# Kernel tuning notes

Measured on AMD Instinct MI355X. Metric: run time of the kernel, lower is better.

Reference implementation:

```python
import jax, jax.numpy as jnp
import numpy as np

DT = 0.001  # integration time step (forward arg dt in the original module)


def force_fn(x):
    # Harmonic well stand-in for the user-supplied force function.
    return -x


def _nh_step(x, v, alpha, kT, mass, Q):
    """One Nose-Hoover step, exactly mirroring the recompute block in backward()."""
    ndof = x.shape[-1]
    v2 = (v * v).sum(-1)
    alpha = alpha + (DT / 4) * (v2 - ndof * kT) / Q
    v = v * jnp.exp(-alpha[..., None] * (DT / 2))
    v2 = (v * v).sum(-1)
    alpha = alpha + (DT / 4) * (v2 - ndof * kT) / Q
    v = v + (DT / 2) * force_fn(x) / mass
    x = x + DT * v
    v = v + (DT / 2) * force_fn(x) / mass
    v2 = (v * v).sum(-1)
    alpha = alpha + (DT / 4) * (v2 - ndof * kT) / Q
    v = v * jnp.exp(-alpha[..., None] * (DT / 2))
    v2 = (v * v).sum(-1)
    alpha = alpha + (DT / 4) * (v2 - ndof * kT) / Q
    return x, v, alpha


def setup_inputs() -> dict:
    key = jax.random.key(0)
    k1, k2 = jax.random.split(key)
    B, D = 4096, 64  # batch of systems, degrees of freedom per system
    return {
        "x0": jax.random.normal(k1, (B, D), jnp.float32),
        "v0": jax.random.normal(k2, (B, D), jnp.float32),
        "alpha0": jnp.zeros((B,), jnp.float32),
        "kT": jnp.ones((), jnp.float32),
        "mass": jnp.ones((), jnp.float32),
        "Q": jnp.ones((), jnp.float32),
        "n_steps": 1000,
        "store_every": 10,
    }


def reference(x0, v0, alpha0, kT, mass, Q, n_steps, store_every):
    n_chunks = n_steps // store_every  # assume divisibility (1000 / 10)

    def inner(c, _):
        x, v, a = c
        return _nh_step(x, v, a, kT, mass, Q), None

    def chunk(c, _):
        c, _ = jax.lax.scan(inner, c, None, length=store_every)
        return c, (c[0], c[1])  # snapshot (x, v) every store_every steps

    _, (xs, vs) = jax.lax.scan(chunk, (x0, v0, alpha0), None, length=n_chunks)
    traj_x = jnp.concatenate([x0[None], xs], axis=0)  # [n_steps//store_every + 1, B, D]
    traj_v = jnp.concatenate([v0[None], vs], axis=0)
    return traj_x, traj_v
```

## Files before the change

### kernel.cpp

```cpp
#include <hip/hip_runtime.h>

#define DT 0.001f

typedef float f4 __attribute__((ext_vector_type(4)));

template<int CTRL>
__device__ __forceinline__ float dpp_add(float v) {
    int r = __builtin_amdgcn_update_dpp(0, __float_as_int(v), CTRL, 0xf, 0xf, false);
    return v + __int_as_float(r);
}

__device__ __forceinline__ float reduce16(float t) {
    t = dpp_add<0x121>(t);
    t = dpp_add<0x122>(t);
    t = dpp_add<0x124>(t);
    t = dpp_add<0x128>(t);
    return t;
}

__device__ __forceinline__ float sumsq(const f4 a) {
    return (a.x * a.x + a.y * a.y) + (a.z * a.z + a.w * a.w);
}
__device__ __forceinline__ float dot4(const f4 a, const f4 b) {
    return (a.x * b.x + a.y * b.y) + (a.z * b.z + a.w * b.w);
}

template<int SE>
__device__ __forceinline__ void run(
    f4& x, f4& u, float& sv, float& al_mcE,
    float& Sxx, float& Sxv, float& Svv,
    int n_chunks, int se_rt,
    float c, float c2, float c2E,
    float A11, float A21,
    float A11sq, float A11A21, float A212, float TWOA11, float TWOA21,
    float Ph1, float Ph2, float Pf1, float Pf2, float kc1, float kc2,
    f4* outx, f4* outv, int snap4, int fidx)
{
    const int se = (SE > 0) ? SE : se_rt;
    float m00 = 1.f, m01 = 0.f, m10 = 0.f, m11 = 1.f;
    float q0 = A11, q1 = 0.f, p0 = A21, p1 = 0.f;
    float e0 = A212 * Sxx, e1 = TWOA21 * Sxv;
    for (int ck = 1; ck <= n_chunks; ++ck) {
        #pragma unroll
        for (int i = 0; i < se - 1; ++i) {
            const float b = sv * DT;
            const float d = sv * A11;
            const float r  = __builtin_fmaf(d, __builtin_fmaf(d, Svv, e1), e0);
            const float a3 = __builtin_fmaf(c, r, al_mcE);
            const float k0 = __builtin_fmaf(c2, r, -c2E);
            const float k1 = __builtin_fmaf(r, kc1, 1.0f);
            const float k2 = r * kc2;
            const float a4 = __builtin_fmaf(a3, __builtin_fmaf(a3, k2, k1), k0);
            const float w  = a3 + a4;
            const float svn = __builtin_fmaf(w, __builtin_fmaf(w, Ph2, Ph1), 1.0f);
            const float sv2 = svn * svn;
            const float cr  = c * r;
            al_mcE = __builtin_fmaf(cr, sv2, a4 - c2E);
            const float n00 = __builtin_fmaf(b, m10, q0);
            const float n01 = __builtin_fmaf(b, m11, q1);
            const float n10 = __builtin_fmaf(d, m10, p0);
            const float n11 = __builtin_fmaf(d, m11, p1);
            m00 = n00; m01 = n01; m10 = n10; m11 = n11;
            q0 = A11 * m00; q1 = A11 * m01;
            p0 = A21 * m00; p1 = A21 * m01;
            const float bb = b * b, bd = b * d;
            const float tb = TWOA11 * b;
            const float mid = __builtin_fmaf(A21, b, A11 * d);
            const float nSxx = __builtin_fmaf(bb, Svv,
                                __builtin_fmaf(tb, Sxv, A11sq * Sxx));
            const float nSxv = __builtin_fmaf(bd, Svv,
                                __builtin_fmaf(mid, Sxv, A11A21 * Sxx));
            Sxx = nSxx; Sxv = nSxv; Svv = r;
            e0 = A212 * Sxx; e1 = TWOA21 * Sxv;
            sv = svn;
        }
        {
            const float b = sv * DT;
            const float d = sv * A11;
            const float r  = __builtin_fmaf(d, __builtin_fmaf(d, Svv, e1), e0);
            const float n00 = __builtin_fmaf(b, m10, q0);
            const float n01 = __builtin_fmaf(b, m11, q1);
            const float n10 = __builtin_fmaf(d, m10, p0);
            const float n11 = __builtin_fmaf(d, m11, p1);
            const float a3 = __builtin_fmaf(c, r, al_mcE);
            const float s2  = __builtin_fmaf(a3, __builtin_fmaf(a3, Ph2, Ph1), 1.0f);
            const float s2q = __builtin_fmaf(a3, __builtin_fmaf(a3, Pf2, Pf1), 1.0f);
            f4 xe = n00 * x + n01 * u;
            f4 ue = n10 * x + n11 * u;
            f4 vs = s2 * ue;
            __builtin_nontemporal_store(xe, &outx[(size_t)ck * snap4 + fidx]);
            __builtin_nontemporal_store(vs, &outv[(size_t)ck * snap4 + fidx]);
            const float Rxx = reduce16(sumsq(xe));
            const float Rxv = reduce16(dot4(xe, vs));
            const float Rvv = reduce16(sumsq(vs));
            const float r2 = r * s2q;
            const float a4 = __builtin_fmaf(c2, r2, a3 - c2E);
            const float s1  = __builtin_fmaf(a4, __builtin_fmaf(a4, Ph2, Ph1), 1.0f);
            const float s1q = __builtin_fmaf(a4, __builtin_fmaf(a4, Pf2, Pf1), 1.0f);
            const float r3 = r2 * s1q;
            al_mcE = __builtin_fmaf(c, r3, a4 - c2E);
            sv = s1;
            x = xe; u = vs;
            Sxx = Rxx; Sxv = Rxv; Svv = Rvv;
            e0 = A212 * Sxx; e1 = TWOA21 * Sxv;
            m00 = 1.f; m01 = 0.f; m10 = 0.f; m11 = 1.f;
            q0 = A11; q1 = 0.f; p0 = A21; p1 = 0.f;
        }
    }
}

__global__ __launch_bounds__(256) void nh_kernel(
    const float* __restrict__ x0, const float* __restrict__ v0,
    const float* __restrict__ alpha0,
    const float* __restrict__ kT_p, const float* __restrict__ mass_p,
    const float* __restrict__ Q_p,
    const int* __restrict__ n_steps_p, const int* __restrict__ store_every_p,
    float* __restrict__ out, int B)
{
    const int D = 64;
    const int gid = blockIdx.x * blockDim.x + threadIdx.x;
    const int sys = gid >> 4;
    const int g   = gid & 15;
    if (sys >= B) return;

    const int n_steps = *n_steps_p;
    const int se      = *store_every_p;
    const int n_chunks = n_steps / se;

    const float kt = *kT_p, m = *mass_p, q = *Q_p;
    const float c   = 0.25f * DT / q;
    const float E   = (float)D * kt;
    const float cE  = c * E;
    const float c2  = 2.0f * c;
    const float c2E = 2.0f * cE;
    const float hd  = 0.5f * DT / m;
    const float hdt = 0.5f * DT;

    const float A11 = 1.0f - hd * DT;
    const float A21 = -hd * (2.0f - hd * DT);
    const float A11sq  = A11 * A11;
    const float A11A21 = A11 * A21;
    const float A212   = A21 * A21;
    const float TWOA11 = 2.0f * A11;
    const float TWOA21 = 2.0f * A21;
    const float Ph1 = -hdt, Ph2 = 0.5f * hdt * hdt;
    const float Pf1 = -DT,  Pf2 = 0.5f * DT * DT;
    const float kc1 = -c2 * DT;
    const float kc2 = 0.5f * c2 * DT * DT;

    const int snap4 = B * 16;
    const int fidx  = sys * 16 + g;

    f4 x = ((const f4*)x0)[fidx];
    f4 v = ((const f4*)v0)[fidx];
    const float al0 = alpha0[sys];

    f4* outx = (f4*)out;
    f4* outv = ((f4*)out) + (size_t)(n_chunks + 1) * snap4;

    __builtin_nontemporal_store(x, &outx[fidx]);
    __builtin_nontemporal_store(v, &outv[fidx]);

    float Svv = reduce16(sumsq(v));
    float Sxx = reduce16(sumsq(x));
    float Sxv = reduce16(dot4(x, v));

    const float a1  = __builtin_fmaf(c, Svv, al0 - cE);
    const float s1  = __builtin_fmaf(a1, __builtin_fmaf(a1, Ph2, Ph1), 1.0f);
    const float s1q = __builtin_fmaf(a1, __builtin_fmaf(a1, Pf2, Pf1), 1.0f);
    float sv = s1;
    const float r1 = Svv * s1q;
    float al_mcE = __builtin_fmaf(c, r1, a1 - c2E);
    f4 u = v;

    if (se == 10)
        run<10>(x, u, sv, al_mcE, Sxx, Sxv, Svv, n_chunks, se, c, c2, c2E,
                A11, A21, A11sq, A11A21, A212, TWOA11, TWOA21,
                Ph1, Ph2, Pf1, Pf2, kc1, kc2, outx, outv, snap4, fidx);
    else
        run<0>(x, u, sv, al_mcE, Sxx, Sxv, Svv, n_chunks, se, c, c2, c2E,
               A11, A21, A11sq, A11A21, A212, TWOA11, TWOA21,
               Ph1, Ph2, Pf1, Pf2, kc1, kc2, outx, outv, snap4, fidx);
}

extern "C" void kernel_launch(void* const* d_in, const int* in_sizes, int n_in,
                              void* d_out, int out_size, void* d_ws, size_t ws_size,
                              hipStream_t stream) {
    const float* x0     = (const float*)d_in[0];
    const float* v0     = (const float*)d_in[1];
    const float* alpha0 = (const float*)d_in[2];
    const float* kT     = (const float*)d_in[3];
    const float* mass   = (const float*)d_in[4];
    const float* Q      = (const float*)d_in[5];
    const int* n_steps  = (const int*)d_in[6];
    const int* store_ev = (const int*)d_in[7];

    const int B = in_sizes[0] / 64;
    const int threads = B * 16;
    const int block = 256;
    const int grid = (threads + block - 1) / block;

    nh_kernel<<<grid, block, 0, stream>>>(x0, v0, alpha0, kT, mass, Q,
                                          n_steps, store_ev, (float*)d_out, B);
}
```

Before: 269.0 us.

## Compute step energy from chunk-start Gram stats via accumulated transfer matrix

Inside each chunk, the kinetic energy r is now computed as a quadratic form of the accumulated 2x2 transfer matrix (n10, n11) against the chunk-start Gram statistics. Before, the Sxx/Sxv/Svv moments were propagated every step. The alpha/scale recurrence is also refolded into precomputed G constants, and the chunk-end update is restructured around the freshly reduced Rvv. The aim is to shorten the serial dependency chain and cut per-step FMA count in this latency-bound scalar recurrence. The cost is a changed float association order, which can shift numerics slightly.

```diff
diff --git a/kernel.cpp b/kernel.cpp
--- a/kernel.cpp
+++ b/kernel.cpp
@@ -27,62 +27,54 @@
 
 template<int SE>
 __device__ __forceinline__ void run(
-    f4& x, f4& u, float& sv, float& al_mcE,
-    float& Sxx, float& Sxv, float& Svv,
+    f4& x, f4& u, float& sv, float& alm,
+    float Sxx0, float tSxv0, float Svv0,
     int n_chunks, int se_rt,
-    float c, float c2, float c2E,
+    float c, float c2, float cE, float c2E, float M2C2E,
     float A11, float A21,
-    float A11sq, float A11A21, float A212, float TWOA11, float TWOA21,
-    float Ph1, float Ph2, float Pf1, float Pf2, float kc1, float kc2,
+    float G00, float G01, float G10, float G11, float G2P,
+    float kc1, float kc2,
+    float Ph1, float Ph2, float Pf1, float Pf2,
     f4* outx, f4* outv, int snap4, int fidx)
 {
     const int se = (SE > 0) ? SE : se_rt;
     float m00 = 1.f, m01 = 0.f, m10 = 0.f, m11 = 1.f;
     float q0 = A11, q1 = 0.f, p0 = A21, p1 = 0.f;
-    float e0 = A212 * Sxx, e1 = TWOA21 * Sxv;
     for (int ck = 1; ck <= n_chunks; ++ck) {
         #pragma unroll
         for (int i = 0; i < se - 1; ++i) {
             const float b = sv * DT;
             const float d = sv * A11;
-            const float r  = __builtin_fmaf(d, __builtin_fmaf(d, Svv, e1), e0);
-            const float a3 = __builtin_fmaf(c, r, al_mcE);
-            const float k0 = __builtin_fmaf(c2, r, -c2E);
-            const float k1 = __builtin_fmaf(r, kc1, 1.0f);
-            const float k2 = r * kc2;
-            const float a4 = __builtin_fmaf(a3, __builtin_fmaf(a3, k2, k1), k0);
-            const float w  = a3 + a4;
-            const float svn = __builtin_fmaf(w, __builtin_fmaf(w, Ph2, Ph1), 1.0f);
-            const float sv2 = svn * svn;
-            const float cr  = c * r;
-            al_mcE = __builtin_fmaf(cr, sv2, a4 - c2E);
             const float n00 = __builtin_fmaf(b, m10, q0);
             const float n01 = __builtin_fmaf(b, m11, q1);
             const float n10 = __builtin_fmaf(d, m10, p0);
             const float n11 = __builtin_fmaf(d, m11, p1);
+            const float u1 = __builtin_fmaf(tSxv0, n11, Sxx0 * n10);
+            const float r  = __builtin_fmaf(Svv0, n11 * n11, n10 * u1);
+            const float a3 = __builtin_fmaf(c, r, alm);
+            const float g0 = __builtin_fmaf(G01, r, G00);
+            const float g1 = __builtin_fmaf(G11, r, G10);
+            const float svn = __builtin_fmaf(a3, __builtin_fmaf(a3, G2P, g1), g0);
+            const float k0m = __builtin_fmaf(c2, r, M2C2E);
+            const float k1  = __builtin_fmaf(kc1, r, 1.0f);
+            const float k2  = kc2 * r;
+            const float a4m = __builtin_fmaf(a3, __builtin_fmaf(a3, k2, k1), k0m);
+            alm = __builtin_fmaf(c * r, svn * svn, a4m);
             m00 = n00; m01 = n01; m10 = n10; m11 = n11;
-            q0 = A11 * m00; q1 = A11 * m01;
-            p0 = A21 * m00; p1 = A21 * m01;
-            const float bb = b * b, bd = b * d;
-            const float tb = TWOA11 * b;
-            const float mid = __builtin_fmaf(A21, b, A11 * d);
-            const float nSxx = __builtin_fmaf(bb, Svv,
-                                __builtin_fmaf(tb, Sxv, A11sq * Sxx));
-            const float nSxv = __builtin_fmaf(bd, Svv,
-                                __builtin_fmaf(mid, Sxv, A11A21 * Sxx));
-            Sxx = nSxx; Sxv = nSxv; Svv = r;
-            e0 = A212 * Sxx; e1 = TWOA21 * Sxv;
+            q0 = A11 * n00; q1 = A11 * n01;
+            p0 = A21 * n00; p1 = A21 * n01;
             sv = svn;
         }
         {
             const float b = sv * DT;
             const float d = sv * A11;
-            const float r  = __builtin_fmaf(d, __builtin_fmaf(d, Svv, e1), e0);
             const float n00 = __builtin_fmaf(b, m10, q0);
             const float n01 = __builtin_fmaf(b, m11, q1);
             const float n10 = __builtin_fmaf(d, m10, p0);
             const float n11 = __builtin_fmaf(d, m11, p1);
-            const float a3 = __builtin_fmaf(c, r, al_mcE);
+            const float u1 = __builtin_fmaf(tSxv0, n11, Sxx0 * n10);
+            const float r  = __builtin_fmaf(Svv0, n11 * n11, n10 * u1);
+            const float a3 = __builtin_fmaf(c, r, alm);
             const float s2  = __builtin_fmaf(a3, __builtin_fmaf(a3, Ph2, Ph1), 1.0f);
             const float s2q = __builtin_fmaf(a3, __builtin_fmaf(a3, Pf2, Pf1), 1.0f);
             f4 xe = n00 * x + n01 * u;
@@ -93,16 +85,15 @@
             const float Rxx = reduce16(sumsq(xe));
             const float Rxv = reduce16(dot4(xe, vs));
             const float Rvv = reduce16(sumsq(vs));
-            const float r2 = r * s2q;
-            const float a4 = __builtin_fmaf(c2, r2, a3 - c2E);
-            const float s1  = __builtin_fmaf(a4, __builtin_fmaf(a4, Ph2, Ph1), 1.0f);
-            const float s1q = __builtin_fmaf(a4, __builtin_fmaf(a4, Pf2, Pf1), 1.0f);
-            const float r3 = r2 * s1q;
-            al_mcE = __builtin_fmaf(c, r3, a4 - c2E);
+            const float r2  = r * s2q;
+            const float aU4 = __builtin_fmaf(c, r2, a3 - cE);
+            const float aU1 = __builtin_fmaf(c, Rvv, aU4 - cE);
+            const float s1  = __builtin_fmaf(aU1, __builtin_fmaf(aU1, Ph2, Ph1), 1.0f);
+            const float s1q = __builtin_fmaf(aU1, __builtin_fmaf(aU1, Pf2, Pf1), 1.0f);
+            alm = __builtin_fmaf(c * Rvv, s1q, aU1 - c2E);
             sv = s1;
             x = xe; u = vs;
-            Sxx = Rxx; Sxv = Rxv; Svv = Rvv;
-            e0 = A212 * Sxx; e1 = TWOA21 * Sxv;
+            Sxx0 = Rxx; tSxv0 = 2.0f * Rxv; Svv0 = Rvv;
             m00 = 1.f; m01 = 0.f; m10 = 0.f; m11 = 1.f;
             q0 = A11; q1 = 0.f; p0 = A21; p1 = 0.f;
         }
@@ -133,20 +124,21 @@
     const float cE  = c * E;
     const float c2  = 2.0f * c;
     const float c2E = 2.0f * cE;
+    const float M2C2E = -2.0f * c2E;
     const float hd  = 0.5f * DT / m;
     const float hdt = 0.5f * DT;
 
     const float A11 = 1.0f - hd * DT;
     const float A21 = -hd * (2.0f - hd * DT);
-    const float A11sq  = A11 * A11;
-    const float A11A21 = A11 * A21;
-    const float A212   = A21 * A21;
-    const float TWOA11 = 2.0f * A11;
-    const float TWOA21 = 2.0f * A21;
     const float Ph1 = -hdt, Ph2 = 0.5f * hdt * hdt;
     const float Pf1 = -DT,  Pf2 = 0.5f * DT * DT;
     const float kc1 = -c2 * DT;
     const float kc2 = 0.5f * c2 * DT * DT;
+    const float G00 = 1.0f - Ph1 * c2E;
+    const float G01 = Ph1 * c2;
+    const float G10 = 2.0f * Ph1;
+    const float G11 = Ph1 * kc1;
+    const float G2P = 4.0f * Ph2;
 
     const int snap4 = B * 16;
     const int fidx  = sys * 16 + g;
@@ -170,17 +162,19 @@
     const float s1q = __builtin_fmaf(a1, __builtin_fmaf(a1, Pf2, Pf1), 1.0f);
     float sv = s1;
     const float r1 = Svv * s1q;
-    float al_mcE = __builtin_fmaf(c, r1, a1 - c2E);
+    float alm = __builtin_fmaf(c, r1, a1 - c2E);
     f4 u = v;
 
     if (se == 10)
-        run<10>(x, u, sv, al_mcE, Sxx, Sxv, Svv, n_chunks, se, c, c2, c2E,
-                A11, A21, A11sq, A11A21, A212, TWOA11, TWOA21,
-                Ph1, Ph2, Pf1, Pf2, kc1, kc2, outx, outv, snap4, fidx);
+        run<10>(x, u, sv, alm, Sxx, 2.0f * Sxv, Svv, n_chunks, se,
+                c, c2, cE, c2E, M2C2E, A11, A21,
+                G00, G01, G10, G11, G2P, kc1, kc2,
+                Ph1, Ph2, Pf1, Pf2, outx, outv, snap4, fidx);
     else
-        run<0>(x, u, sv, al_mcE, Sxx, Sxv, Svv, n_chunks, se, c, c2, c2E,
-               A11, A21, A11sq, A11A21, A212, TWOA11, TWOA21,
-               Ph1, Ph2, Pf1, Pf2, kc1, kc2, outx, outv, snap4, fidx);
+        run<0>(x, u, sv, alm, Sxx, 2.0f * Sxv, Svv, n_chunks, se,
+               c, c2, cE, c2E, M2C2E, A11, A21,
+               G00, G01, G10, G11, G2P, kc1, kc2,
+               Ph1, Ph2, Pf1, Pf2, outx, outv, snap4, fidx);
 }
 
 extern "C" void kernel_launch(void* const* d_in, const int* in_sizes, int n_in,
```

Measured after the change: 256.6 us. 4.6% less time.
